# Kernel optimization log

Measured on AMD Instinct MI355X. Metric: run time of the kernel, lower is better.

Reference implementation:

```python
import jax, jax.numpy as jnp
import numpy as np

EPS = 1e-12


def setup_inputs() -> dict:
    key = jax.random.key(0)
    k1, k2 = jax.random.split(key)
    batch, seq_len, hidden, conv_size = 64, 4096, 128, 16
    input_tensor = jax.random.normal(k1, (batch, seq_len, hidden), dtype=jnp.float32)
    conv_weight = jax.random.normal(k2, (1, conv_size, hidden), dtype=jnp.float32) * 0.02
    ln_weight = jnp.ones((hidden,), dtype=jnp.float32)
    ln_bias = jnp.zeros((hidden,), dtype=jnp.float32)
    return {"input_tensor": input_tensor, "conv_weight": conv_weight,
            "ln_weight": ln_weight, "ln_bias": ln_bias}


def reference(input_tensor, conv_weight, ln_weight, ln_bias):
    # input_tensor: [B, S, H]; conv_weight: [1, K, H] zero-padded to length S
    seq_len = input_tensor.shape[1]
    x = jnp.fft.rfft(input_tensor, axis=1, norm="ortho")  # [B, S//2+1, H] complex
    pad = seq_len - conv_weight.shape[1]
    w = jnp.pad(conv_weight, ((0, 0), (0, pad), (0, 0)))
    w = jnp.fft.rfft(w, axis=1, norm="ortho")  # [1, S//2+1, H]
    y = jnp.fft.irfft(x * w, n=seq_len, axis=1, norm="ortho")  # [B, S, H]
    # dropout is identity at inference; residual + TF-style LayerNorm
    h = y + input_tensor
    u = h.mean(-1, keepdims=True)
    s = ((h - u) ** 2).mean(-1, keepdims=True)
    return ln_weight * (h - u) / jnp.sqrt(s + EPS) + ln_bias
```

## Files before the change

### kernel.cpp

```cpp
#include <hip/hip_runtime.h>


constexpr int S = 4096;
constexpr int H = 128;
constexpr int K = 16;
constexpr int CHUNK = 32;
constexpr int G = 8;

typedef float v2f __attribute__((ext_vector_type(2)));

template <int CTRL, int ROWMASK>
__device__ __forceinline__ float dpp_add(float x) {
    int y = __builtin_amdgcn_update_dpp(0, __float_as_int(x), CTRL, ROWMASK, 0xf, true);
    return x + __int_as_float(y);
}

__device__ __forceinline__ float wave_sum(float x) {
    x = dpp_add<0x111, 0xf>(x);
    x = dpp_add<0x112, 0xf>(x);
    x = dpp_add<0x114, 0xf>(x);
    x = dpp_add<0x118, 0xf>(x);
    x = dpp_add<0x142, 0xa>(x);
    x = dpp_add<0x143, 0xc>(x);
    return __int_as_float(__builtin_amdgcn_readlane(__float_as_int(x), 63));
}

__global__ __launch_bounds__(256, 4)
void fconv_ln_kernel(const float* __restrict__ x,
                     const float* __restrict__ wconv,
                     const float* __restrict__ lnw,
                     const float* __restrict__ lnb,
                     float* __restrict__ out)
{
    const int wid  = (blockIdx.x * blockDim.x + threadIdx.x) >> 6;
    const int lane = threadIdx.x & 63;

    const int chunksPerSeq = S / CHUNK;
    const int b  = wid / chunksPerSeq;
    const int t0 = (wid % chunksPerSeq) * CHUNK;

    const int c2 = lane * 2;

    float2 w[K];
#pragma unroll
    for (int k = 0; k < K; ++k)
        w[k] = *reinterpret_cast<const float2*>(&wconv[k * H + c2]);

    const float2 gamma = *reinterpret_cast<const float2*>(&lnw[c2]);
    const float2 beta  = *reinterpret_cast<const float2*>(&lnb[c2]);

    const float* xb = x   + (size_t)b * S * H;
    float*       ob = out + (size_t)b * S * H;

    float2 hist[K];
    float2 cur[G];
    float2 nxt[G];

#pragma unroll
    for (int s = 0; s < K; ++s) {
        int t = (t0 - K + s + S) & (S - 1);
        hist[s] = *reinterpret_cast<const float2*>(&xb[(size_t)t * H + c2]);
    }
#pragma unroll
    for (int j = 0; j < G; ++j)
        cur[j] = *reinterpret_cast<const float2*>(&xb[(size_t)(t0 + j) * H + c2]);

    for (int tb = 0; tb < CHUNK; tb += G) {
        if (tb + G < CHUNK) {
#pragma unroll
            for (int j = 0; j < G; ++j)
                nxt[j] = *reinterpret_cast<const float2*>(
                    &xb[(size_t)(t0 + tb + G + j) * H + c2]);
        }

#pragma unroll
        for (int j = 0; j < G; ++j) {
            float ax = 0.f, ay = 0.f;
#pragma unroll
            for (int k = 0; k < K; ++k) {
                const float2 v = (k <= j) ? cur[j - k] : hist[K + j - k];
                ax = fmaf(w[k].x, v.x, ax);
                ay = fmaf(w[k].y, v.y, ay);
            }
            const float2 xt = cur[j];
            float hx = fmaf(ax, 0.015625f, xt.x);
            float hy = fmaf(ay, 0.015625f, xt.y);

            const float s1 = wave_sum(hx + hy);
            const float s2 = wave_sum(hx * hx + hy * hy);
            const float u   = s1 * (1.0f / H);
            const float var = fmaf(s2, 1.0f / H, -u * u);
            const float inv = rsqrtf(var + 1e-12f);

            v2f o;
            o.x = fmaf(gamma.x * inv, hx - u, beta.x);
            o.y = fmaf(gamma.y * inv, hy - u, beta.y);
            __builtin_nontemporal_store(
                o, reinterpret_cast<v2f*>(&ob[(size_t)(t0 + tb + j) * H + c2]));
        }

#pragma unroll
        for (int s = 0; s < K - G; ++s) hist[s] = hist[s + G];
#pragma unroll
        for (int j = 0; j < G; ++j)     hist[K - G + j] = cur[j];
#pragma unroll
        for (int j = 0; j < G; ++j)     cur[j] = nxt[j];
    }
}

extern "C" void kernel_launch(void* const* d_in, const int* in_sizes, int n_in,
                              void* d_out, int out_size, void* d_ws, size_t ws_size,
                              hipStream_t stream)
{
    const float* x     = (const float*)d_in[0];
    const float* wconv = (const float*)d_in[1];
    const float* lnw   = (const float*)d_in[2];
    const float* lnb   = (const float*)d_in[3];
    float*       out   = (float*)d_out;

    const int Bsz = in_sizes[0] / (S * H);
    const int totalWaves = Bsz * (S / CHUNK);
    const int threads = 256;
    const int blocks  = totalWaves * 64 / threads;

    hipLaunchKernelGGL(fconv_ln_kernel, dim3(blocks), dim3(threads), 0, stream,
                       x, wconv, lnw, lnb, out);
}
```

Baseline: 242.1 us.

## Stage input tile in LDS via async global_load_lds shared across block waves

Each 256-thread block now covers 64 timesteps and loads the 80-row tile (64 rows plus the 16-row causal halo) into shared memory with asynchronous global-to-LDS copies. Each wave then works on 16 rows from LDS using a register ring buffer. Previously every wave reloaded its own 16-row halo from global memory for a 32-row chunk. The change cuts redundant halo reads and load instructions. In exchange it adds an LDS round-trip, a block barrier, and a serialized load-then-compute phase with no overlap inside a block, and it drops the occupancy hint in launch bounds.

After: 237.8 us. About the same (-1.8%).

```diff
diff --git a/kernel.cpp b/kernel.cpp
--- a/kernel.cpp
+++ b/kernel.cpp
@@ -4,10 +4,17 @@
 constexpr int S = 4096;
 constexpr int H = 128;
 constexpr int K = 16;
-constexpr int CHUNK = 32;
-constexpr int G = 8;
+constexpr int TB = 64;
+constexpr int ROWS = TB + K;
+constexpr int NCHUNK = ROWS / 2;
 
 typedef float v2f __attribute__((ext_vector_type(2)));
+typedef const void __attribute__((address_space(1))) gas_v;
+typedef void __attribute__((address_space(3))) las_v;
+
+__device__ __forceinline__ void async_copy16(const float* gsrc, float* ldst) {
+    __builtin_amdgcn_global_load_lds((gas_v*)gsrc, (las_v*)ldst, 16, 0, 0);
+}
 
 template <int CTRL, int ROWMASK>
 __device__ __forceinline__ float dpp_add(float x) {
@@ -25,86 +32,81 @@
     return __int_as_float(__builtin_amdgcn_readlane(__float_as_int(x), 63));
 }
 
-__global__ __launch_bounds__(256, 4)
+__global__ __launch_bounds__(256)
 void fconv_ln_kernel(const float* __restrict__ x,
                      const float* __restrict__ wconv,
                      const float* __restrict__ lnw,
                      const float* __restrict__ lnb,
                      float* __restrict__ out)
 {
-    const int wid  = (blockIdx.x * blockDim.x + threadIdx.x) >> 6;
+    __shared__ float tile[ROWS * H];
+
+    const int wv   = threadIdx.x >> 6;
     const int lane = threadIdx.x & 63;
 
-    const int chunksPerSeq = S / CHUNK;
-    const int b  = wid / chunksPerSeq;
-    const int t0 = (wid % chunksPerSeq) * CHUNK;
+    const int chunksPerSeq = S / TB;
+    const int b  = blockIdx.x / chunksPerSeq;
+    const int t0 = (blockIdx.x % chunksPerSeq) * TB;
 
     const int c2 = lane * 2;
+
+    const float* xb = x   + (size_t)b * S * H;
+    float*       ob = out + (size_t)b * S * H;
 
     float2 w[K];
 #pragma unroll
     for (int k = 0; k < K; ++k)
         w[k] = *reinterpret_cast<const float2*>(&wconv[k * H + c2]);
-
     const float2 gamma = *reinterpret_cast<const float2*>(&lnw[c2]);
     const float2 beta  = *reinterpret_cast<const float2*>(&lnb[c2]);
 
-    const float* xb = x   + (size_t)b * S * H;
-    float*       ob = out + (size_t)b * S * H;
+    {
+        const int rsub = lane >> 5;
+        const int coff = (lane & 31) * 4;
+#pragma unroll
+        for (int i = 0; i < NCHUNK / 4; ++i) {
+            const int c  = wv * (NCHUNK / 4) + i;
+            const int rr = 2 * c + rsub;
+            const int gt = (t0 - K + rr) & (S - 1);
+            async_copy16(xb + (size_t)gt * H + coff, &tile[c * 256]);
+        }
+    }
+    asm volatile("s_waitcnt vmcnt(0)" ::: "memory");
+    __syncthreads();
 
-    float2 hist[K];
-    float2 cur[G];
-    float2 nxt[G];
+    const int start = wv * 16;
+    float2 ring[K];
+#pragma unroll
+    for (int m = 1; m <= 15; ++m)
+        ring[m] = *reinterpret_cast<const float2*>(&tile[(start + m) * H + c2]);
 
 #pragma unroll
-    for (int s = 0; s < K; ++s) {
-        int t = (t0 - K + s + S) & (S - 1);
-        hist[s] = *reinterpret_cast<const float2*>(&xb[(size_t)t * H + c2]);
-    }
+    for (int j = 0; j < 16; ++j) {
+        ring[j & 15] = *reinterpret_cast<const float2*>(
+            &tile[(start + 16 + j) * H + c2]);
+
+        float ax = 0.f, ay = 0.f;
 #pragma unroll
-    for (int j = 0; j < G; ++j)
-        cur[j] = *reinterpret_cast<const float2*>(&xb[(size_t)(t0 + j) * H + c2]);
+        for (int k = 0; k < K; ++k) {
+            const float2 v = ring[(j + 16 - k) & 15];
+            ax = fmaf(w[k].x, v.x, ax);
+            ay = fmaf(w[k].y, v.y, ay);
+        }
+        const float2 xt = ring[j & 15];
+        float hx = fmaf(ax, 0.015625f, xt.x);
+        float hy = fmaf(ay, 0.015625f, xt.y);
 
-    for (int tb = 0; tb < CHUNK; tb += G) {
-        if (tb + G < CHUNK) {
-#pragma unroll
-            for (int j = 0; j < G; ++j)
-                nxt[j] = *reinterpret_cast<const float2*>(
-                    &xb[(size_t)(t0 + tb + G + j) * H + c2]);
-        }
+        const float s1 = wave_sum(hx + hy);
+        const float s2 = wave_sum(hx * hx + hy * hy);
+        const float u   = s1 * (1.0f / H);
+        const float var = fmaf(s2, 1.0f / H, -u * u);
+        const float inv = rsqrtf(var + 1e-12f);
 
-#pragma unroll
-        for (int j = 0; j < G; ++j) {
-            float ax = 0.f, ay = 0.f;
-#pragma unroll
-            for (int k = 0; k < K; ++k) {
-                const float2 v = (k <= j) ? cur[j - k] : hist[K + j - k];
-                ax = fmaf(w[k].x, v.x, ax);
-                ay = fmaf(w[k].y, v.y, ay);
-            }
-            const float2 xt = cur[j];
-            float hx = fmaf(ax, 0.015625f, xt.x);
-            float hy = fmaf(ay, 0.015625f, xt.y);
-
-            const float s1 = wave_sum(hx + hy);
-            const float s2 = wave_sum(hx * hx + hy * hy);
-            const float u   = s1 * (1.0f / H);
-            const float var = fmaf(s2, 1.0f / H, -u * u);
-            const float inv = rsqrtf(var + 1e-12f);
-
-            v2f o;
-            o.x = fmaf(gamma.x * inv, hx - u, beta.x);
-            o.y = fmaf(gamma.y * inv, hy - u, beta.y);
-            __builtin_nontemporal_store(
-                o, reinterpret_cast<v2f*>(&ob[(size_t)(t0 + tb + j) * H + c2]));
-        }
-
-#pragma unroll
-        for (int s = 0; s < K - G; ++s) hist[s] = hist[s + G];
-#pragma unroll
-        for (int j = 0; j < G; ++j)     hist[K - G + j] = cur[j];
-#pragma unroll
-        for (int j = 0; j < G; ++j)     cur[j] = nxt[j];
+        v2f o;
+        o.x = fmaf(gamma.x * inv, hx - u, beta.x);
+        o.y = fmaf(gamma.y * inv, hy - u, beta.y);
+        __builtin_nontemporal_store(
+            o, reinterpret_cast<v2f*>(&ob[(size_t)(t0 + start + j) * H + c2]));
     }
 }
 
@@ -118,11 +120,8 @@
     const float* lnb   = (const float*)d_in[3];
     float*       out   = (float*)d_out;
 
-    const int Bsz = in_sizes[0] / (S * H);
-    const int totalWaves = Bsz * (S / CHUNK);
-    const int threads = 256;
-    const int blocks  = totalWaves * 64 / threads;
-
-    hipLaunchKernelGGL(fconv_ln_kernel, dim3(blocks), dim3(threads), 0, stream,
+    const int Bsz    = in_sizes[0] / (S * H);
+    const int blocks = Bsz * (S / TB);
+    hipLaunchKernelGGL(fconv_ln_kernel, dim3(blocks), dim3(256), 0, stream,
                        x, wconv, lnw, lnb, out);
 }
```
